# Performance work log

Hardware: AMD Instinct MI355X
Metric: run time of the kernel (lower is better)

Reference implementation:

```python
import jax, jax.numpy as jnp
import numpy as np

E, D, H, K, N = 8, 512, 2048, 2, 1024  # experts, d_model, d_hidden, top_k, tokens
EPS = 1e-5


def _moe_linear(x, idx, W, b):
    # x: (M, in); idx: (M,) expert id per row; W: (E, out, in); b: (E, out)
    # Brute-force: compute per-expert dense GEMMs, select via one-hot (matches
    # BruteForceMoELinear math: y[i] = x[i] @ W[idx[i]].T + b[idx[i]]).
    m = jax.nn.one_hot(idx, W.shape[0], dtype=x.dtype)  # (M, E)
    y = jnp.einsum('me,eoi,mi->mo', m, W, x)
    return y + jnp.take(b, idx, axis=0)


def _forward(inp, gate_w, gate_b, w1, b1, w2, b2, ln_w, ln_b):
    # NaiveGate: linear -> top_k -> softmax over top-k logits
    logits = inp @ gate_w.T + gate_b              # (N, E)
    top_val, top_idx = jax.lax.top_k(logits, K)   # (N, K)
    score = jax.nn.softmax(top_val, axis=-1)      # (N, K)
    # repeat_interleave tokens, dispatch to experts
    x = jnp.repeat(inp, K, axis=0)                # (N*K, D)
    idx = top_idx.reshape(-1)                     # (N*K,)
    x = _moe_linear(x, idx, w1, b1)               # (N*K, H)
    x = jax.nn.gelu(x, approximate=False)         # torch F.gelu default = erf
    x = _moe_linear(x, idx, w2, b2)               # (N*K, D)
    x = x.reshape(N, K, D)
    x = jnp.einsum('nk,nkd->nd', score, x)        # bmm((N,1,K),(N,K,D)) combine
    # post layer norm (pre_lnorm=False)
    mu = jnp.mean(x, axis=-1, keepdims=True)
    var = jnp.var(x, axis=-1, keepdims=True)
    return (x - mu) * jax.lax.rsqrt(var + EPS) * ln_w + ln_b


def setup_inputs() -> dict:
    key = jax.random.key(0)
    ks = jax.random.split(key, 8)
    s = 0.02
    return {
        'inp': jax.random.normal(ks[0], (N, D), dtype=jnp.float32),
        'gate_w': s * jax.random.normal(ks[1], (E, D), dtype=jnp.float32),
        'gate_b': jnp.zeros((E,), dtype=jnp.float32),
        'w1': s * jax.random.normal(ks[2], (E, H, D), dtype=jnp.float32),
        'b1': jnp.zeros((E, H), dtype=jnp.float32),
        'w2': s * jax.random.normal(ks[3], (E, D, H), dtype=jnp.float32),
        'b2': jnp.zeros((E, D), dtype=jnp.float32),
        'ln_w': jnp.ones((D,), dtype=jnp.float32),
        'ln_b': jnp.zeros((D,), dtype=jnp.float32),
    }


def reference(inp, gate_w, gate_b, w1, b1, w2, b2, ln_w, ln_b):
    return _forward(inp, gate_w, gate_b, w1, b1, w2, b2, ln_w, ln_b)
```

## Files before the change

kernel.cpp:

```cpp
#include <hip/hip_runtime.h>
#include <cstdint>
#include <cstddef>

typedef _Float16 half_t;
typedef _Float16 half8 __attribute__((ext_vector_type(8)));
typedef float floatx4 __attribute__((ext_vector_type(4)));

#define E_ 8
#define D_ 512
#define H_ 2048
#define NTOK 1024
#define NP 2048
#define TM 64
#define MAX_TILES 40

__device__ __forceinline__ float gelu_f(float x) {
    return 0.5f * x * (1.0f + erff(x * 0.7071067811865476f));
}

__device__ __forceinline__ void gload_lds16(const half_t* g, half_t* l) {
    __builtin_amdgcn_global_load_lds(
        (__attribute__((address_space(1))) void*)(g),
        (__attribute__((address_space(3))) void*)(l),
        16, 0, 0);
}

__global__ __launch_bounds__(256) void gate_kernel(
        const float* __restrict__ inp, const float* __restrict__ gate_w,
        const float* __restrict__ gate_b, float* __restrict__ logits) {
    int n = blockIdx.x * 4 + (threadIdx.x >> 6);
    int lane = threadIdx.x & 63;
    const floatx4* xr = (const floatx4*)(inp + (size_t)n * D_);
    floatx4 x0 = xr[lane * 2], x1 = xr[lane * 2 + 1];
    #pragma unroll
    for (int e = 0; e < E_; e++) {
        const floatx4* gr = (const floatx4*)(gate_w + (size_t)e * D_);
        floatx4 g0 = gr[lane * 2], g1 = gr[lane * 2 + 1];
        float p = x0[0]*g0[0] + x0[1]*g0[1] + x0[2]*g0[2] + x0[3]*g0[3]
                + x1[0]*g1[0] + x1[1]*g1[1] + x1[2]*g1[2] + x1[3]*g1[3];
        #pragma unroll
        for (int m = 1; m < 64; m <<= 1) p += __shfl_xor(p, m);
        if (lane == 0) logits[(size_t)n * E_ + e] = p + gate_b[e];
    }
}

__global__ __launch_bounds__(256) void plan_kernel(
        const float* __restrict__ logits, float* __restrict__ score,
        int* __restrict__ idx, int* __restrict__ pos_of_pair,
        int* __restrict__ tile_e, int* __restrict__ tile_row0,
        int* __restrict__ tile_cnt, int* __restrict__ ntiles) {
    __shared__ int cnt_s[E_], off_s[E_ + 1], cur_s[E_];
    int tid = threadIdx.x;
    if (tid < E_) { cnt_s[tid] = 0; cur_s[tid] = 0; }
    __syncthreads();
    int my_e[4][2];
    #pragma unroll
    for (int i = 0; i < 4; i++) {
        int n = tid + i * 256;
        float l[E_];
        #pragma unroll
        for (int e = 0; e < E_; e++) l[e] = logits[(size_t)n * E_ + e];
        int e0 = 0; float v0 = l[0];
        #pragma unroll
        for (int e = 1; e < E_; e++) if (l[e] > v0) { v0 = l[e]; e0 = e; }
        int e1 = -1; float v1 = -3.4e38f;
        #pragma unroll
        for (int e = 0; e < E_; e++) if (e != e0 && l[e] > v1) { v1 = l[e]; e1 = e; }
        float s1 = expf(v1 - v0);
        float den = 1.0f + s1;
        score[2 * n]     = 1.0f / den;
        score[2 * n + 1] = s1 / den;
        idx[2 * n]     = e0;
        idx[2 * n + 1] = e1;
        atomicAdd(&cnt_s[e0], 1);
        atomicAdd(&cnt_s[e1], 1);
        my_e[i][0] = e0; my_e[i][1] = e1;
    }
    __syncthreads();
    if (tid == 0) {
        int o = 0;
        #pragma unroll
        for (int e = 0; e < E_; e++) { off_s[e] = o; o += cnt_s[e]; }
        off_s[E_] = o;
        int t = 0;
        for (int e = 0; e < E_; e++) {
            int c = cnt_s[e];
            int nt = (c + TM - 1) / TM;
            for (int i = 0; i < nt; i++) {
                tile_e[t] = e;
                tile_row0[t] = off_s[e] + i * TM;
                int rem = c - i * TM;
                tile_cnt[t] = rem < TM ? rem : TM;
                t++;
            }
        }
        ntiles[0] = t;
    }
    __syncthreads();
    #pragma unroll
    for (int i = 0; i < 4; i++) {
        #pragma unroll
        for (int k = 0; k < 2; k++) {
            int p = (tid + i * 256) * 2 + k;
            int e = my_e[i][k];
            int r = atomicAdd(&cur_s[e], 1);
            pos_of_pair[p] = off_s[e] + r;
        }
    }
}

__global__ __launch_bounds__(256) void scatter_kernel(
        const float* __restrict__ inp, const int* __restrict__ pos_of_pair,
        half_t* __restrict__ Xg) {
    int p = blockIdx.x * 4 + (threadIdx.x >> 6);
    int lane = threadIdx.x & 63;
    int pos = pos_of_pair[p];
    int n = p >> 1;
    const floatx4* src = (const floatx4*)(inp + (size_t)n * D_);
    floatx4 f0 = src[lane * 2], f1 = src[lane * 2 + 1];
    half8 h = { (half_t)f0[0], (half_t)f0[1], (half_t)f0[2], (half_t)f0[3],
                (half_t)f1[0], (half_t)f1[1], (half_t)f1[2], (half_t)f1[3] };
    *(half8*)(Xg + (size_t)pos * D_ + lane * 8) = h;
}

__global__ __launch_bounds__(256) void cvt_kernel(
        const float* __restrict__ w1, const float* __restrict__ w2,
        half_t* __restrict__ W1h, half_t* __restrict__ W2h) {
    const int n8 = E_ * H_ * D_ / 8;
    int i = blockIdx.x * 256 + threadIdx.x;
    const float* src; half_t* dst; int j;
    if (i < n8) { src = w1; dst = W1h; j = i; }
    else        { src = w2; dst = W2h; j = i - n8; }
    const floatx4* s = (const floatx4*)src + (size_t)j * 2;
    floatx4 f0 = s[0], f1 = s[1];
    half8 h = { (half_t)f0[0], (half_t)f0[1], (half_t)f0[2], (half_t)f0[3],
                (half_t)f1[0], (half_t)f1[1], (half_t)f1[2], (half_t)f1[3] };
    *(half8*)(dst + (size_t)j * 8) = h;
}

__global__ __launch_bounds__(256) void gemm1_kernel(
        const half_t* __restrict__ Xg, const half_t* __restrict__ W1h,
        const float* __restrict__ b1,
        const int* __restrict__ tile_e, const int* __restrict__ tile_row0,
        const int* __restrict__ tile_cnt, const int* __restrict__ ntiles,
        half_t* __restrict__ Y1) {
    __shared__ half_t As[2][TM * 64];
    __shared__ half_t Bs[2][128 * 64];
    int t = blockIdx.x;
    if (t >= ntiles[0]) return;
    int e = tile_e[t], row0 = tile_row0[t], cnt = tile_cnt[t];
    int colbase = blockIdx.y * 128;
    int tid = threadIdx.x;
    int wave = tid >> 6, lane = tid & 63;
    int quad = lane >> 4, l16 = lane & 15;
    int wm = (wave & 1) * 32, wn = (wave >> 1) * 64;

    int srow = tid >> 3, skc = (tid & 7) * 8;
    const half_t* Ag0 = Xg + (size_t)(row0 + srow) * D_ + skc;
    const half_t* Ag1 = Ag0 + 32 * D_;
    const half_t* Bg0 = W1h + ((size_t)e * H_ + colbase + srow) * D_ + skc;
    const half_t* Bg1 = Bg0 + 32 * D_;
    const half_t* Bg2 = Bg0 + 64 * D_;
    const half_t* Bg3 = Bg0 + 96 * D_;

    #define STAGE1(buf, k0)                                        \
        do {                                                       \
            gload_lds16(Ag0 + (k0), &As[buf][(size_t)tid * 8]);            \
            gload_lds16(Ag1 + (k0), &As[buf][(size_t)(tid + 256) * 8]);    \
            gload_lds16(Bg0 + (k0), &Bs[buf][(size_t)tid * 8]);            \
            gload_lds16(Bg1 + (k0), &Bs[buf][(size_t)(tid + 256) * 8]);    \
            gload_lds16(Bg2 + (k0), &Bs[buf][(size_t)(tid + 512) * 8]);    \
            gload_lds16(Bg3 + (k0), &Bs[buf][(size_t)(tid + 768) * 8]);    \
        } while (0)

    floatx4 acc[2][4] = {};
    STAGE1(0, 0);
    __syncthreads();
    int cur = 0;
    for (int k0 = 0; k0 < D_; k0 += 64) {
        if (k0 + 64 < D_) STAGE1(cur ^ 1, k0 + 64);
        const half_t* Ab = &As[cur][0];
        const half_t* Bb = &Bs[cur][0];
        #pragma unroll
        for (int ks = 0; ks < 2; ks++) {
            half8 a[2], b[4];
            #pragma unroll
            for (int mi = 0; mi < 2; mi++)
                a[mi] = *(const half8*)(Ab + (wm + mi * 16 + l16) * 64 + ks * 32 + quad * 8);
            #pragma unroll
            for (int ni = 0; ni < 4; ni++)
                b[ni] = *(const half8*)(Bb + (wn + ni * 16 + l16) * 64 + ks * 32 + quad * 8);
            #pragma unroll
            for (int mi = 0; mi < 2; mi++)
                #pragma unroll
                for (int ni = 0; ni < 4; ni++)
                    acc[mi][ni] = __builtin_amdgcn_mfma_f32_16x16x32_f16(a[mi], b[ni], acc[mi][ni], 0, 0, 0);
        }
        __syncthreads();
        cur ^= 1;
    }
    #undef STAGE1

    float bias[4];
    #pragma unroll
    for (int ni = 0; ni < 4; ni++)
        bias[ni] = b1[(size_t)e * H_ + colbase + wn + ni * 16 + l16];
    #pragma unroll
    for (int mi = 0; mi < 2; mi++) {
        #pragma unroll
        for (int r = 0; r < 4; r++) {
            int rr = wm + mi * 16 + quad * 4 + r;
            if (rr >= cnt) continue;
            size_t rowoff = (size_t)(row0 + rr) * H_;
            #pragma unroll
            for (int ni = 0; ni < 4; ni++) {
                float v = acc[mi][ni][r] + bias[ni];
                Y1[rowoff + colbase + wn + ni * 16 + l16] = (half_t)gelu_f(v);
            }
        }
    }
}

__global__ __launch_bounds__(256) void gemm2_kernel(
        const half_t* __restrict__ Y1, const half_t* __restrict__ W2h,
        const int* __restrict__ tile_e, const int* __restrict__ tile_row0,
        const int* __restrict__ tile_cnt, const int* __restrict__ ntiles,
        float* __restrict__ Y2p) {
    __shared__ half_t As[2][TM * 64];
    __shared__ half_t Bs[2][128 * 64];
    int t = blockIdx.x;
    if (t >= ntiles[0]) return;
    int e = tile_e[t], row0 = tile_row0[t], cnt = tile_cnt[t];
    int colbase = blockIdx.y * 128;
    int kz = blockIdx.z;
    int kzbase = kz * 512;
    int tid = threadIdx.x;
    int wave = tid >> 6, lane = tid & 63;
    int quad = lane >> 4, l16 = lane & 15;
    int wm = (wave & 1) * 32, wn = (wave >> 1) * 64;

    int srow = tid >> 3, skc = (tid & 7) * 8;
    const half_t* Ag0 = Y1 + (size_t)(row0 + srow) * H_ + kzbase + skc;
    const half_t* Ag1 = Ag0 + 32 * H_;
    const half_t* Bg0 = W2h + ((size_t)e * D_ + colbase + srow) * H_ + kzbase + skc;
    const half_t* Bg1 = Bg0 + 32 * H_;
    const half_t* Bg2 = Bg0 + 64 * H_;
    const half_t* Bg3 = Bg0 + 96 * H_;

    #define STAGE2(buf, k0)                                        \
        do {                                                       \
            gload_lds16(Ag0 + (k0), &As[buf][(size_t)tid * 8]);            \
            gload_lds16(Ag1 + (k0), &As[buf][(size_t)(tid + 256) * 8]);    \
            gload_lds16(Bg0 + (k0), &Bs[buf][(size_t)tid * 8]);            \
            gload_lds16(Bg1 + (k0), &Bs[buf][(size_t)(tid + 256) * 8]);    \
            gload_lds16(Bg2 + (k0), &Bs[buf][(size_t)(tid + 512) * 8]);    \
            gload_lds16(Bg3 + (k0), &Bs[buf][(size_t)(tid + 768) * 8]);    \
        } while (0)

    floatx4 acc[2][4] = {};
    STAGE2(0, 0);
    __syncthreads();
    int cur = 0;
    for (int k0 = 0; k0 < 512; k0 += 64) {
        if (k0 + 64 < 512) STAGE2(cur ^ 1, k0 + 64);
        const half_t* Ab = &As[cur][0];
        const half_t* Bb = &Bs[cur][0];
        #pragma unroll
        for (int ks = 0; ks < 2; ks++) {
            half8 a[2], b[4];
            #pragma unroll
            for (int mi = 0; mi < 2; mi++)
                a[mi] = *(const half8*)(Ab + (wm + mi * 16 + l16) * 64 + ks * 32 + quad * 8);
            #pragma unroll
            for (int ni = 0; ni < 4; ni++)
                b[ni] = *(const half8*)(Bb + (wn + ni * 16 + l16) * 64 + ks * 32 + quad * 8);
            #pragma unroll
            for (int mi = 0; mi < 2; mi++)
                #pragma unroll
                for (int ni = 0; ni < 4; ni++)
                    acc[mi][ni] = __builtin_amdgcn_mfma_f32_16x16x32_f16(a[mi], b[ni], acc[mi][ni], 0, 0, 0);
        }
        __syncthreads();
        cur ^= 1;
    }
    #undef STAGE2

    #pragma unroll
    for (int mi = 0; mi < 2; mi++) {
        #pragma unroll
        for (int r = 0; r < 4; r++) {
            int rr = wm + mi * 16 + quad * 4 + r;
            if (rr >= cnt) continue;
            size_t rowoff = ((size_t)kz * NP + row0 + rr) * D_;
            #pragma unroll
            for (int ni = 0; ni < 4; ni++)
                Y2p[rowoff + colbase + wn + ni * 16 + l16] = acc[mi][ni][r];
        }
    }
}

__global__ __launch_bounds__(256) void final_kernel(
        const float* __restrict__ Y2p, const float* __restrict__ b2,
        const int* __restrict__ idx, const float* __restrict__ score,
        const int* __restrict__ pos_of_pair,
        const float* __restrict__ ln_w, const float* __restrict__ ln_b,
        float* __restrict__ out) {
    int n = blockIdx.x * 4 + (threadIdx.x >> 6);
    int lane = threadIdx.x & 63;
    int p0 = pos_of_pair[2 * n], p1 = pos_of_pair[2 * n + 1];
    int e0 = idx[2 * n], e1 = idx[2 * n + 1];
    float s0 = score[2 * n], s1 = score[2 * n + 1];

    const floatx4* b2r0 = (const floatx4*)(b2 + (size_t)e0 * D_);
    const floatx4* b2r1 = (const floatx4*)(b2 + (size_t)e1 * D_);
    floatx4 a_lo = b2r0[lane * 2], a_hi = b2r0[lane * 2 + 1];
    floatx4 c_lo = b2r1[lane * 2], c_hi = b2r1[lane * 2 + 1];
    #pragma unroll
    for (int kz = 0; kz < 4; kz++) {
        const floatx4* r0 = (const floatx4*)(Y2p + ((size_t)kz * NP + p0) * D_);
        const floatx4* r1 = (const floatx4*)(Y2p + ((size_t)kz * NP + p1) * D_);
        a_lo += r0[lane * 2]; a_hi += r0[lane * 2 + 1];
        c_lo += r1[lane * 2]; c_hi += r1[lane * 2 + 1];
    }
    floatx4 y_lo = s0 * a_lo + s1 * c_lo;
    floatx4 y_hi = s0 * a_hi + s1 * c_hi;

    float s = 0.0f, q = 0.0f;
    #pragma unroll
    for (int j = 0; j < 4; j++) {
        s += y_lo[j] + y_hi[j];
        q += y_lo[j] * y_lo[j] + y_hi[j] * y_hi[j];
    }
    #pragma unroll
    for (int m = 1; m < 64; m <<= 1) {
        s += __shfl_xor(s, m);
        q += __shfl_xor(q, m);
    }
    float mean = s * (1.0f / 512.0f);
    float var = q * (1.0f / 512.0f) - mean * mean;
    float inv = 1.0f / sqrtf(var + 1e-5f);

    const floatx4* wv = (const floatx4*)ln_w;
    const floatx4* bv = (const floatx4*)ln_b;
    floatx4 o_lo = (y_lo - mean) * inv * wv[lane * 2]     + bv[lane * 2];
    floatx4 o_hi = (y_hi - mean) * inv * wv[lane * 2 + 1] + bv[lane * 2 + 1];
    floatx4* op = (floatx4*)(out + (size_t)n * D_);
    op[lane * 2] = o_lo;
    op[lane * 2 + 1] = o_hi;
}

extern "C" void kernel_launch(void* const* d_in, const int* in_sizes, int n_in,
                              void* d_out, int out_size, void* d_ws, size_t ws_size,
                              hipStream_t stream) {
    const float* inp    = (const float*)d_in[0];
    const float* gate_w = (const float*)d_in[1];
    const float* gate_b = (const float*)d_in[2];
    const float* w1     = (const float*)d_in[3];
    const float* b1     = (const float*)d_in[4];
    const float* w2     = (const float*)d_in[5];
    const float* b2     = (const float*)d_in[6];
    const float* ln_w   = (const float*)d_in[7];
    const float* ln_b   = (const float*)d_in[8];
    float* out = (float*)d_out;

    char* ws = (char*)d_ws;
    size_t o = 0;
    auto carve = [&](size_t bytes) -> char* {
        char* p = ws + o;
        o += (bytes + 255) & ~(size_t)255;
        return p;
    };
    half_t* W1h = (half_t*)carve(sizeof(half_t) * (size_t)E_ * H_ * D_);
    half_t* W2h = (half_t*)carve(sizeof(half_t) * (size_t)E_ * D_ * H_);
    half_t* Xg  = (half_t*)carve(sizeof(half_t) * (size_t)(NP + 128) * D_);
    half_t* Y1  = (half_t*)carve(sizeof(half_t) * (size_t)(NP + 128) * H_);
    float*  Y2p = (float*)carve(sizeof(float) * 4 * (size_t)NP * D_);
    float*  logits = (float*)carve(sizeof(float) * NTOK * E_);
    float*  score  = (float*)carve(sizeof(float) * NP);
    int* idx         = (int*)carve(sizeof(int) * NP);
    int* pos_of_pair = (int*)carve(sizeof(int) * NP);
    int* tile_e      = (int*)carve(sizeof(int) * MAX_TILES);
    int* tile_row0   = (int*)carve(sizeof(int) * MAX_TILES);
    int* tile_cnt    = (int*)carve(sizeof(int) * MAX_TILES);
    int* ntiles      = (int*)carve(sizeof(int) * 1);

    gate_kernel<<<NTOK / 4, 256, 0, stream>>>(inp, gate_w, gate_b, logits);
    plan_kernel<<<1, 256, 0, stream>>>(logits, score, idx, pos_of_pair,
                                       tile_e, tile_row0, tile_cnt, ntiles);
    scatter_kernel<<<NP / 4, 256, 0, stream>>>(inp, pos_of_pair, Xg);
    cvt_kernel<<<2 * E_ * H_ * D_ / 8 / 256, 256, 0, stream>>>(w1, w2, W1h, W2h);
    gemm1_kernel<<<dim3(MAX_TILES, H_ / 128), 256, 0, stream>>>(
        Xg, W1h, b1, tile_e, tile_row0, tile_cnt, ntiles, Y1);
    gemm2_kernel<<<dim3(MAX_TILES, D_ / 128, 4), 256, 0, stream>>>(
        Y1, W2h, tile_e, tile_row0, tile_cnt, ntiles, Y2p);
    final_kernel<<<NTOK / 4, 256, 0, stream>>>(Y2p, b2, idx, score, pos_of_pair, ln_w, ln_b, out);
}
```

Baseline: 171.8 us.

## Fuse fp32-to-fp16 weight conversion into MoE GEMM loaders and swizzle LDS

Drops the separate weight-conversion kernel. Both expert GEMMs now read fp32 weights straight from global memory into registers, convert them to fp16 and write them into LDS with an XOR swizzle, prefetching one k-step ahead. Activation tiles use the same XOR swizzle through the direct-to-LDS path, which should cut LDS bank conflicts on fragment reads. This removes a full pass that read and wrote all the weights, at the cost of register staging and more global traffic, since each weight tile is re-read as fp32 by every token tile of the same expert.

```diff
diff --git a/kernel.cpp b/kernel.cpp
--- a/kernel.cpp
+++ b/kernel.cpp
@@ -123,28 +123,13 @@
     *(half8*)(Xg + (size_t)pos * D_ + lane * 8) = h;
 }
 
-__global__ __launch_bounds__(256) void cvt_kernel(
-        const float* __restrict__ w1, const float* __restrict__ w2,
-        half_t* __restrict__ W1h, half_t* __restrict__ W2h) {
-    const int n8 = E_ * H_ * D_ / 8;
-    int i = blockIdx.x * 256 + threadIdx.x;
-    const float* src; half_t* dst; int j;
-    if (i < n8) { src = w1; dst = W1h; j = i; }
-    else        { src = w2; dst = W2h; j = i - n8; }
-    const floatx4* s = (const floatx4*)src + (size_t)j * 2;
-    floatx4 f0 = s[0], f1 = s[1];
-    half8 h = { (half_t)f0[0], (half_t)f0[1], (half_t)f0[2], (half_t)f0[3],
-                (half_t)f1[0], (half_t)f1[1], (half_t)f1[2], (half_t)f1[3] };
-    *(half8*)(dst + (size_t)j * 8) = h;
-}
-
 __global__ __launch_bounds__(256) void gemm1_kernel(
-        const half_t* __restrict__ Xg, const half_t* __restrict__ W1h,
+        const half_t* __restrict__ Xg, const float* __restrict__ w1,
         const float* __restrict__ b1,
         const int* __restrict__ tile_e, const int* __restrict__ tile_row0,
         const int* __restrict__ tile_cnt, const int* __restrict__ ntiles,
         half_t* __restrict__ Y1) {
-    __shared__ half_t As[2][TM * 64];
+    __shared__ half_t As[2][64 * 64];
     __shared__ half_t Bs[2][128 * 64];
     int t = blockIdx.x;
     if (t >= ntiles[0]) return;
@@ -154,31 +139,44 @@
     int wave = tid >> 6, lane = tid & 63;
     int quad = lane >> 4, l16 = lane & 15;
     int wm = (wave & 1) * 32, wn = (wave >> 1) * 64;
-
-    int srow = tid >> 3, skc = (tid & 7) * 8;
-    const half_t* Ag0 = Xg + (size_t)(row0 + srow) * D_ + skc;
+    int xm = l16 & 7;
+
+    int gr = tid >> 3, gc = tid & 7;
+    int gsw = gc ^ (gr & 7);
+
+    const half_t* Ag0 = Xg + (size_t)(row0 + gr) * D_ + gsw * 8;
     const half_t* Ag1 = Ag0 + 32 * D_;
-    const half_t* Bg0 = W1h + ((size_t)e * H_ + colbase + srow) * D_ + skc;
-    const half_t* Bg1 = Bg0 + 32 * D_;
-    const half_t* Bg2 = Bg0 + 64 * D_;
-    const half_t* Bg3 = Bg0 + 96 * D_;
-
-    #define STAGE1(buf, k0)                                        \
-        do {                                                       \
-            gload_lds16(Ag0 + (k0), &As[buf][(size_t)tid * 8]);            \
-            gload_lds16(Ag1 + (k0), &As[buf][(size_t)(tid + 256) * 8]);    \
-            gload_lds16(Bg0 + (k0), &Bs[buf][(size_t)tid * 8]);            \
-            gload_lds16(Bg1 + (k0), &Bs[buf][(size_t)(tid + 256) * 8]);    \
-            gload_lds16(Bg2 + (k0), &Bs[buf][(size_t)(tid + 512) * 8]);    \
-            gload_lds16(Bg3 + (k0), &Bs[buf][(size_t)(tid + 768) * 8]);    \
-        } while (0)
+    const float* Bg = w1 + ((size_t)e * H_ + colbase + gr) * D_ + gc * 8;
+    int bslot = gr * 64 + gsw * 8;
+
+    floatx4 br0[4], br1[4];
+
+    #define STAGEA1(buf, k0) do { \
+        gload_lds16(Ag0 + (k0), &As[buf][(size_t)tid * 8]); \
+        gload_lds16(Ag1 + (k0), &As[buf][(size_t)(tid + 256) * 8]); } while (0)
+
+    #define LOADB1(k0) do { \
+        _Pragma("unroll") \
+        for (int i = 0; i < 4; i++) { \
+            const floatx4* p = (const floatx4*)(Bg + (size_t)i * 32 * D_ + (k0)); \
+            br0[i] = p[0]; br1[i] = p[1]; } } while (0)
+
+    #define CVTWRB1(buf) do { \
+        _Pragma("unroll") \
+        for (int i = 0; i < 4; i++) { \
+            half8 h = { (half_t)br0[i][0], (half_t)br0[i][1], (half_t)br0[i][2], (half_t)br0[i][3], \
+                        (half_t)br1[i][0], (half_t)br1[i][1], (half_t)br1[i][2], (half_t)br1[i][3] }; \
+            *(half8*)(&Bs[buf][bslot + i * 2048]) = h; } } while (0)
 
     floatx4 acc[2][4] = {};
-    STAGE1(0, 0);
+    STAGEA1(0, 0);
+    LOADB1(0);
+    CVTWRB1(0);
     __syncthreads();
     int cur = 0;
     for (int k0 = 0; k0 < D_; k0 += 64) {
-        if (k0 + 64 < D_) STAGE1(cur ^ 1, k0 + 64);
+        bool more = (k0 + 64) < D_;
+        if (more) { STAGEA1(cur ^ 1, k0 + 64); LOADB1(k0 + 64); }
         const half_t* Ab = &As[cur][0];
         const half_t* Bb = &Bs[cur][0];
         #pragma unroll
@@ -186,20 +184,23 @@
             half8 a[2], b[4];
             #pragma unroll
             for (int mi = 0; mi < 2; mi++)
-                a[mi] = *(const half8*)(Ab + (wm + mi * 16 + l16) * 64 + ks * 32 + quad * 8);
+                a[mi] = *(const half8*)(Ab + (wm + mi * 16 + l16) * 64 + ((ks * 4 + quad) ^ xm) * 8);
             #pragma unroll
             for (int ni = 0; ni < 4; ni++)
-                b[ni] = *(const half8*)(Bb + (wn + ni * 16 + l16) * 64 + ks * 32 + quad * 8);
+                b[ni] = *(const half8*)(Bb + (wn + ni * 16 + l16) * 64 + ((ks * 4 + quad) ^ xm) * 8);
             #pragma unroll
             for (int mi = 0; mi < 2; mi++)
                 #pragma unroll
                 for (int ni = 0; ni < 4; ni++)
                     acc[mi][ni] = __builtin_amdgcn_mfma_f32_16x16x32_f16(a[mi], b[ni], acc[mi][ni], 0, 0, 0);
         }
+        if (more) CVTWRB1(cur ^ 1);
         __syncthreads();
         cur ^= 1;
     }
-    #undef STAGE1
+    #undef STAGEA1
+    #undef LOADB1
+    #undef CVTWRB1
 
     float bias[4];
     #pragma unroll
@@ -222,11 +223,11 @@
 }
 
 __global__ __launch_bounds__(256) void gemm2_kernel(
-        const half_t* __restrict__ Y1, const half_t* __restrict__ W2h,
+        const half_t* __restrict__ Y1, const float* __restrict__ w2,
         const int* __restrict__ tile_e, const int* __restrict__ tile_row0,
         const int* __restrict__ tile_cnt, const int* __restrict__ ntiles,
         float* __restrict__ Y2p) {
-    __shared__ half_t As[2][TM * 64];
+    __shared__ half_t As[2][64 * 64];
     __shared__ half_t Bs[2][128 * 64];
     int t = blockIdx.x;
     if (t >= ntiles[0]) return;
@@ -238,31 +239,44 @@
     int wave = tid >> 6, lane = tid & 63;
     int quad = lane >> 4, l16 = lane & 15;
     int wm = (wave & 1) * 32, wn = (wave >> 1) * 64;
-
-    int srow = tid >> 3, skc = (tid & 7) * 8;
-    const half_t* Ag0 = Y1 + (size_t)(row0 + srow) * H_ + kzbase + skc;
+    int xm = l16 & 7;
+
+    int gr = tid >> 3, gc = tid & 7;
+    int gsw = gc ^ (gr & 7);
+
+    const half_t* Ag0 = Y1 + (size_t)(row0 + gr) * H_ + kzbase + gsw * 8;
     const half_t* Ag1 = Ag0 + 32 * H_;
-    const half_t* Bg0 = W2h + ((size_t)e * D_ + colbase + srow) * H_ + kzbase + skc;
-    const half_t* Bg1 = Bg0 + 32 * H_;
-    const half_t* Bg2 = Bg0 + 64 * H_;
-    const half_t* Bg3 = Bg0 + 96 * H_;
-
-    #define STAGE2(buf, k0)                                        \
-        do {                                                       \
-            gload_lds16(Ag0 + (k0), &As[buf][(size_t)tid * 8]);            \
-            gload_lds16(Ag1 + (k0), &As[buf][(size_t)(tid + 256) * 8]);    \
-            gload_lds16(Bg0 + (k0), &Bs[buf][(size_t)tid * 8]);            \
-            gload_lds16(Bg1 + (k0), &Bs[buf][(size_t)(tid + 256) * 8]);    \
-            gload_lds16(Bg2 + (k0), &Bs[buf][(size_t)(tid + 512) * 8]);    \
-            gload_lds16(Bg3 + (k0), &Bs[buf][(size_t)(tid + 768) * 8]);    \
-        } while (0)
+    const float* Bg = w2 + ((size_t)e * D_ + colbase + gr) * H_ + kzbase + gc * 8;
+    int bslot = gr * 64 + gsw * 8;
+
+    floatx4 br0[4], br1[4];
+
+    #define STAGEA2(buf, k0) do { \
+        gload_lds16(Ag0 + (k0), &As[buf][(size_t)tid * 8]); \
+        gload_lds16(Ag1 + (k0), &As[buf][(size_t)(tid + 256) * 8]); } while (0)
+
+    #define LOADB2(k0) do { \
+        _Pragma("unroll") \
+        for (int i = 0; i < 4; i++) { \
+            const floatx4* p = (const floatx4*)(Bg + (size_t)i * 32 * H_ + (k0)); \
+            br0[i] = p[0]; br1[i] = p[1]; } } while (0)
+
+    #define CVTWRB2(buf) do { \
+        _Pragma("unroll") \
+        for (int i = 0; i < 4; i++) { \
+            half8 h = { (half_t)br0[i][0], (half_t)br0[i][1], (half_t)br0[i][2], (half_t)br0[i][3], \
+                        (half_t)br1[i][0], (half_t)br1[i][1], (half_t)br1[i][2], (half_t)br1[i][3] }; \
+            *(half8*)(&Bs[buf][bslot + i * 2048]) = h; } } while (0)
 
     floatx4 acc[2][4] = {};
-    STAGE2(0, 0);
+    STAGEA2(0, 0);
+    LOADB2(0);
+    CVTWRB2(0);
     __syncthreads();
     int cur = 0;
     for (int k0 = 0; k0 < 512; k0 += 64) {
-        if (k0 + 64 < 512) STAGE2(cur ^ 1, k0 + 64);
+        bool more = (k0 + 64) < 512;
+        if (more) { STAGEA2(cur ^ 1, k0 + 64); LOADB2(k0 + 64); }
         const half_t* Ab = &As[cur][0];
         const half_t* Bb = &Bs[cur][0];
         #pragma unroll
@@ -270,20 +284,23 @@
             half8 a[2], b[4];
             #pragma unroll
             for (int mi = 0; mi < 2; mi++)
-                a[mi] = *(const half8*)(Ab + (wm + mi * 16 + l16) * 64 + ks * 32 + quad * 8);
+                a[mi] = *(const half8*)(Ab + (wm + mi * 16 + l16) * 64 + ((ks * 4 + quad) ^ xm) * 8);
             #pragma unroll
             for (int ni = 0; ni < 4; ni++)
-                b[ni] = *(const half8*)(Bb + (wn + ni * 16 + l16) * 64 + ks * 32 + quad * 8);
+                b[ni] = *(const half8*)(Bb + (wn + ni * 16 + l16) * 64 + ((ks * 4 + quad) ^ xm) * 8);
             #pragma unroll
             for (int mi = 0; mi < 2; mi++)
                 #pragma unroll
                 for (int ni = 0; ni < 4; ni++)
                     acc[mi][ni] = __builtin_amdgcn_mfma_f32_16x16x32_f16(a[mi], b[ni], acc[mi][ni], 0, 0, 0);
         }
+        if (more) CVTWRB2(cur ^ 1);
         __syncthreads();
         cur ^= 1;
     }
-    #undef STAGE2
+    #undef STAGEA2
+    #undef LOADB2
+    #undef CVTWRB2
 
     #pragma unroll
     for (int mi = 0; mi < 2; mi++) {
@@ -370,8 +387,6 @@
         o += (bytes + 255) & ~(size_t)255;
         return p;
     };
-    half_t* W1h = (half_t*)carve(sizeof(half_t) * (size_t)E_ * H_ * D_);
-    half_t* W2h = (half_t*)carve(sizeof(half_t) * (size_t)E_ * D_ * H_);
     half_t* Xg  = (half_t*)carve(sizeof(half_t) * (size_t)(NP + 128) * D_);
     half_t* Y1  = (half_t*)carve(sizeof(half_t) * (size_t)(NP + 128) * H_);
     float*  Y2p = (float*)carve(sizeof(float) * 4 * (size_t)NP * D_);
@@ -388,10 +403,9 @@
     plan_kernel<<<1, 256, 0, stream>>>(logits, score, idx, pos_of_pair,
                                        tile_e, tile_row0, tile_cnt, ntiles);
     scatter_kernel<<<NP / 4, 256, 0, stream>>>(inp, pos_of_pair, Xg);
-    cvt_kernel<<<2 * E_ * H_ * D_ / 8 / 256, 256, 0, stream>>>(w1, w2, W1h, W2h);
     gemm1_kernel<<<dim3(MAX_TILES, H_ / 128), 256, 0, stream>>>(
-        Xg, W1h, b1, tile_e, tile_row0, tile_cnt, ntiles, Y1);
+        Xg, w1, b1, tile_e, tile_row0, tile_cnt, ntiles, Y1);
     gemm2_kernel<<<dim3(MAX_TILES, D_ / 128, 4), 256, 0, stream>>>(
-        Y1, W2h, tile_e, tile_row0, tile_cnt, ntiles, Y2p);
+        Y1, w2, tile_e, tile_row0, tile_cnt, ntiles, Y2p);
     final_kernel<<<NTOK / 4, 256, 0, stream>>>(Y2p, b2, idx, score, pos_of_pair, ln_w, ln_b, out);
 }
```

Measured after the change: 178.0 us. 3.6% more time.
